# Kernel optimization log

Hardware: AMD Instinct MI355X
Metric: run time of the kernel (lower is better)

## Reference

```python
import jax, jax.numpy as jnp
import numpy as np

B, AT, NBR = 8, 96, 512
NG, NT = 25, 5            # n_gaussian_triple, n_theta
NANG = NG * NT            # 125, filternet input dim
NF = 128                  # n_filters
NB = 128                  # n_atom_basis


def ssp(x):
    # shifted softplus: ln(0.5*e^x + 0.5) = softplus(x) - ln(2)
    return jax.nn.softplus(x) - jnp.asarray(np.log(2.0), x.dtype)


def setup_inputs() -> dict:
    key = jax.random.key(0)
    ks = jax.random.split(key, 16)
    s = lambda fan_in: 1.0 / np.sqrt(fan_in)
    return {
        "x": jax.random.normal(ks[0], (B, AT, NB), jnp.float32),
        "triple_ijk": jax.random.uniform(ks[1], (B, AT, NBR, NANG), jnp.float32),
        "neighbors_j": jax.random.randint(ks[2], (B, AT, NBR), 0, AT, jnp.int32),
        "neighbors_k": jax.random.randint(ks[3], (B, AT, NBR), 0, AT, jnp.int32),
        "triple_mask": jnp.ones((B, AT, NBR), jnp.float32),
        # filter network (Dense ssp -> Dense linear)
        "W1": jax.random.normal(ks[4], (NANG, NF), jnp.float32) * s(NANG),
        "b1": jnp.zeros((NF,), jnp.float32),
        "W2": jax.random.normal(ks[5], (NF, NF), jnp.float32) * s(NF),
        "b2": jnp.zeros((NF,), jnp.float32),
        # cfconv in2f (no bias) and f2out (ssp activation)
        "Win": jax.random.normal(ks[6], (NB, NF), jnp.float32) * s(NB),
        "Wf2": jax.random.normal(ks[7], (NF, NB), jnp.float32) * s(NF),
        "bf2": jnp.zeros((NB,), jnp.float32),
        # final dense (linear) before residual
        "Wd": jax.random.normal(ks[8], (NB, NB), jnp.float32) * s(NB),
        "bd": jnp.zeros((NB,), jnp.float32),
    }


def _gather_atoms(y, nbh):
    # y: (B, At, F); nbh: (B, At, Nbr) -> (B, At, Nbr, F)
    b, at, nbr = nbh.shape
    idx = nbh.reshape(b, at * nbr, 1)
    return jnp.take_along_axis(y, idx, axis=1).reshape(b, at, nbr, y.shape[-1])


def reference(x, triple_ijk, neighbors_j, neighbors_k, triple_mask,
              W1, b1, W2, b2, Win, Wf2, bf2, Wd, bd):
    # filter network on angular/radial triple features -> (B, At, Nbr, NF)
    W_triple = ssp(triple_ijk @ W1 + b1) @ W2 + b2
    # in2f
    y = x @ Win                                  # (B, At, NF)
    y_j = _gather_atoms(y, neighbors_j)          # (B, At, Nbr, NF)
    y_k = _gather_atoms(y, neighbors_k)          # (B, At, Nbr, NF)
    # element-wise continuous-filter conv over triples, mask padded triples
    yt = y_j * y_k * W_triple * triple_mask[..., None]
    agg = jnp.sum(yt, axis=2)                    # sum-aggregate over triples
    v = ssp(agg @ Wf2 + bf2)                     # f2out with shifted softplus
    v = v @ Wd + bd                              # interaction dense
    return x + v                                 # residual
```

## Files before the change

kernel.cpp:

```cpp
#include <hip/hip_runtime.h>
#include <math.h>

#define B_    8
#define AT_   96
#define NBR_  512
#define NANG_ 125
#define NF_   128
#define NB_   128
#define TN    32
#define NCHUNK 2
#define CROWS (NBR_ / NCHUNK)
#define NTI   (CROWS / TN)
#define TSTRIDE 136
#define JSTRIDE 132

typedef __attribute__((ext_vector_type(8))) short bf16x8;
typedef __attribute__((ext_vector_type(4))) float f32x4;

__device__ __forceinline__ short f2bf(float f) {
    union { float f; unsigned u; } x; x.f = f;
    return (short)((x.u + 0x8000u) >> 16);
}

__device__ __forceinline__ float sspf(float x) {
    float p = __builtin_amdgcn_exp2f(x * 1.44269504088896340736f);
    float l = __builtin_amdgcn_logf(1.0f + p);
    return 0.69314718055994530942f * l - 0.69314718055994530942f;
}

__device__ __forceinline__ f32x4 ld4u(const float* p) {
    f32x4 v; __builtin_memcpy(&v, p, 16); return v;
}

__device__ __forceinline__ bf16x8 cvt8(f32x4 lo, f32x4 hi) {
    unsigned r0, r1, r2, r3;
    asm("v_cvt_pk_bf16_f32 %0, %1, %2" : "=v"(r0) : "v"(lo.x), "v"(lo.y));
    asm("v_cvt_pk_bf16_f32 %0, %1, %2" : "=v"(r1) : "v"(lo.z), "v"(lo.w));
    asm("v_cvt_pk_bf16_f32 %0, %1, %2" : "=v"(r2) : "v"(hi.x), "v"(hi.y));
    asm("v_cvt_pk_bf16_f32 %0, %1, %2" : "=v"(r3) : "v"(hi.z), "v"(hi.w));
    typedef __attribute__((ext_vector_type(4))) unsigned u32x4;
    u32x4 r = { r0, r1, r2, r3 };
    return __builtin_bit_cast(bf16x8, r);
}

__global__ __launch_bounds__(128) void prep_kernel(
    const float* __restrict__ x, const float* __restrict__ Win,
    const float* __restrict__ W1, const float* __restrict__ W2,
    float* __restrict__ y, short* __restrict__ w1p, short* __restrict__ w2p)
{
    __shared__ float xs[4][NB_];
    int blk = blockIdx.x, tid = threadIdx.x;
    if (blk < 192) {
        int row0 = blk * 4;
        #pragma unroll
        for (int r = 0; r < 4; r++) xs[r][tid] = x[(row0 + r) * NB_ + tid];
        __syncthreads();
        float a0 = 0.f, a1 = 0.f, a2 = 0.f, a3 = 0.f;
        #pragma unroll 8
        for (int k = 0; k < NB_; k++) {
            float w = Win[k * NF_ + tid];
            a0 = fmaf(xs[0][k], w, a0);
            a1 = fmaf(xs[1][k], w, a1);
            a2 = fmaf(xs[2][k], w, a2);
            a3 = fmaf(xs[3][k], w, a3);
        }
        y[(row0 + 0) * NF_ + tid] = a0;
        y[(row0 + 1) * NF_ + tid] = a1;
        y[(row0 + 2) * NF_ + tid] = a2;
        y[(row0 + 3) * NF_ + tid] = a3;
    } else {
        int t = (blk - 192) * 128 + tid;
        int j = t & 7, lane = (t >> 3) & 63, ks = (t >> 9) & 3, ct = t >> 11;
        int k = ks * 32 + (lane >> 4) * 8 + j;
        int n = ct * 16 + (lane & 15);
        w1p[t] = (k < NANG_) ? f2bf(W1[k * NF_ + n]) : (short)0;
        w2p[t] = f2bf(W2[k * NF_ + n]);
    }
}

__global__ __launch_bounds__(256, 2) void triple_partial(
    const float* __restrict__ trip,
    const int* __restrict__ nbj, const int* __restrict__ nbk,
    const float* __restrict__ maskg,
    const float* __restrict__ b1g, const float* __restrict__ b2g,
    const float* __restrict__ y, const short* __restrict__ w1p,
    const short* __restrict__ w2p, float* __restrict__ pagg)
{
    __shared__ short hs[2][TN * TSTRIDE];
    __shared__ float yjk[2][TN * JSTRIDE];

    const int tid = threadIdx.x;
    const int wave = tid >> 6, lane = tid & 63;
    const int quad = lane >> 4, col = lane & 15;
    const int blk = blockIdx.x;
    const int bid = blk >> 1, c = blk & 1;
    const int b = bid / AT_;

    const float* tpc = trip + (long)bid * NBR_ * NANG_ + (long)c * CROWS * NANG_;
    const int nb_base = bid * NBR_ + c * CROWS;

    const int ct0 = 2 * wave, ct1 = 2 * wave + 1;
    const int f0 = ct0 * 16 + col, f1 = ct1 * 16 + col;
    const float bias1_0 = b1g[f0], bias1_1 = b1g[f1];
    const float bias2_0 = b2g[f0], bias2_1 = b2g[f1];

    const int yrow = tid >> 3, ypart = tid & 7;
    const bool lastblk = (blk == B_ * AT_ * NCHUNK - 1);

    bf16x8 w1f0[4], w1f1[4], w2f0[4], w2f1[4];
    #pragma unroll
    for (int ks = 0; ks < 4; ks++) {
        w1f0[ks] = *(const bf16x8*)&w1p[(ct0 * 4 + ks) * 512 + lane * 8];
        w1f1[ks] = *(const bf16x8*)&w1p[(ct1 * 4 + ks) * 512 + lane * 8];
        w2f0[ks] = *(const bf16x8*)&w2p[(ct0 * 4 + ks) * 512 + lane * 8];
        w2f1[ks] = *(const bf16x8*)&w2p[(ct1 * 4 + ks) * 512 + lane * 8];
    }

    int jj = nbj[nb_base + yrow];
    int kk = nbk[nb_base + yrow];
    float mk = maskg[nb_base + yrow];

    const float* arow = tpc + col * NANG_;
    f32x4 pa0 = ld4u(arow + quad * 8);
    f32x4 pa1 = ld4u(arow + quad * 8 + 4);
    f32x4 pb0 = ld4u(arow + 16 * NANG_ + quad * 8);
    f32x4 pb1 = ld4u(arow + 16 * NANG_ + quad * 8 + 4);

    float accw0 = 0.f, accw1 = 0.f;
    int cur = 0;

    for (int nt = 0; nt < NTI; nt++) {
        const float* yjp = y + (b * AT_ + jj) * NF_ + ypart * 16;
        const float* ykp = y + (b * AT_ + kk) * NF_ + ypart * 16;
        f32x4 j0 = ((const f32x4*)yjp)[0], j1 = ((const f32x4*)yjp)[1];
        f32x4 j2 = ((const f32x4*)yjp)[2], j3 = ((const f32x4*)yjp)[3];
        f32x4 k0 = ((const f32x4*)ykp)[0], k1 = ((const f32x4*)ykp)[1];
        f32x4 k2 = ((const f32x4*)ykp)[2], k3 = ((const f32x4*)ykp)[3];
        const float mc = mk;
        if (nt + 1 < NTI) {
            jj = nbj[nb_base + (nt + 1) * TN + yrow];
            kk = nbk[nb_base + (nt + 1) * TN + yrow];
            mk = maskg[nb_base + (nt + 1) * TN + yrow];
        }

        const bool lt = lastblk && (nt == NTI - 1);
        const float* anext = (nt == NTI - 1) ? arow : (arow + TN * NANG_);

        f32x4 d00 = {0,0,0,0}, d01 = {0,0,0,0}, d10 = {0,0,0,0}, d11 = {0,0,0,0};
        #pragma unroll
        for (int ks = 0; ks < 4; ks++) {
            bf16x8 a0 = cvt8(pa0, pa1);
            bf16x8 a1 = cvt8(pb0, pb1);
            const float* pn = (ks < 3) ? arow : anext;
            const int    ko = (ks < 3) ? ((ks + 1) * 32 + quad * 8) : (quad * 8);
            pa0 = ld4u(pn + ko);
            pa1 = ld4u(pn + ko + 4);
            pb0 = ld4u(pn + 16 * NANG_ + ko);
            if (ks == 2 && lt && lane == 63) {
                pb1 = (f32x4){ pn[16 * NANG_ + ko + 4], 0.f, 0.f, 0.f };
            } else {
                pb1 = ld4u(pn + 16 * NANG_ + ko + 4);
            }
            d00 = __builtin_amdgcn_mfma_f32_16x16x32_bf16(a0, w1f0[ks], d00, 0, 0, 0);
            d01 = __builtin_amdgcn_mfma_f32_16x16x32_bf16(a0, w1f1[ks], d01, 0, 0, 0);
            d10 = __builtin_amdgcn_mfma_f32_16x16x32_bf16(a1, w1f0[ks], d10, 0, 0, 0);
            d11 = __builtin_amdgcn_mfma_f32_16x16x32_bf16(a1, w1f1[ks], d11, 0, 0, 0);
        }
        arow = anext;

        {
            float* d = &yjk[cur][yrow * JSTRIDE + ypart * 16];
            *(f32x4*)(d + 0)  = j0 * k0 * mc;
            *(f32x4*)(d + 4)  = j1 * k1 * mc;
            *(f32x4*)(d + 8)  = j2 * k2 * mc;
            *(f32x4*)(d + 12) = j3 * k3 * mc;
        }
        #pragma unroll
        for (int r = 0; r < 4; r++) {
            int row0 = quad * 4 + r, row1 = 16 + quad * 4 + r;
            hs[cur][row0 * TSTRIDE + f0] = f2bf(sspf(d00[r] + bias1_0));
            hs[cur][row0 * TSTRIDE + f1] = f2bf(sspf(d01[r] + bias1_1));
            hs[cur][row1 * TSTRIDE + f0] = f2bf(sspf(d10[r] + bias1_0));
            hs[cur][row1 * TSTRIDE + f1] = f2bf(sspf(d11[r] + bias1_1));
        }
        __syncthreads();

        f32x4 e00 = {0,0,0,0}, e01 = {0,0,0,0}, e10 = {0,0,0,0}, e11 = {0,0,0,0};
        #pragma unroll
        for (int ks = 0; ks < 4; ks++) {
            bf16x8 a0 = *(const bf16x8*)&hs[cur][(     col) * TSTRIDE + ks * 32 + quad * 8];
            bf16x8 a1 = *(const bf16x8*)&hs[cur][(16 + col) * TSTRIDE + ks * 32 + quad * 8];
            e00 = __builtin_amdgcn_mfma_f32_16x16x32_bf16(a0, w2f0[ks], e00, 0, 0, 0);
            e01 = __builtin_amdgcn_mfma_f32_16x16x32_bf16(a0, w2f1[ks], e01, 0, 0, 0);
            e10 = __builtin_amdgcn_mfma_f32_16x16x32_bf16(a1, w2f0[ks], e10, 0, 0, 0);
            e11 = __builtin_amdgcn_mfma_f32_16x16x32_bf16(a1, w2f1[ks], e11, 0, 0, 0);
        }
        #pragma unroll
        for (int r = 0; r < 4; r++) {
            int row0 = quad * 4 + r, row1 = 16 + quad * 4 + r;
            accw0 += (e00[r] + bias2_0) * yjk[cur][row0 * JSTRIDE + f0];
            accw1 += (e01[r] + bias2_1) * yjk[cur][row0 * JSTRIDE + f1];
            accw0 += (e10[r] + bias2_0) * yjk[cur][row1 * JSTRIDE + f0];
            accw1 += (e11[r] + bias2_1) * yjk[cur][row1 * JSTRIDE + f1];
        }
        cur ^= 1;
    }

    accw0 += __shfl_xor(accw0, 16, 64);
    accw0 += __shfl_xor(accw0, 32, 64);
    accw1 += __shfl_xor(accw1, 16, 64);
    accw1 += __shfl_xor(accw1, 32, 64);
    if (quad == 0) {
        pagg[blk * NF_ + f0] = accw0;
        pagg[blk * NF_ + f1] = accw1;
    }
}

__global__ __launch_bounds__(128) void finish_kernel(
    const float* __restrict__ x, const float* __restrict__ pagg,
    const float* __restrict__ Wf2, const float* __restrict__ bf2,
    const float* __restrict__ Wd, const float* __restrict__ bd,
    float* __restrict__ out)
{
    __shared__ float aggs[NF_];
    __shared__ float t1s[NF_];
    int bid = blockIdx.x, f = threadIdx.x;
    float a = pagg[(bid * 2 + 0) * NF_ + f] + pagg[(bid * 2 + 1) * NF_ + f];
    aggs[f] = a;
    __syncthreads();
    float acc = 0.f;
    #pragma unroll 8
    for (int k = 0; k < NF_; k++) acc = fmaf(aggs[k], Wf2[k * NB_ + f], acc);
    t1s[f] = sspf(acc + bf2[f]);
    __syncthreads();
    acc = 0.f;
    #pragma unroll 8
    for (int k = 0; k < NB_; k++) acc = fmaf(t1s[k], Wd[k * NB_ + f], acc);
    out[bid * NB_ + f] = x[bid * NB_ + f] + acc + bd[f];
}

extern "C" void kernel_launch(void* const* d_in, const int* in_sizes, int n_in,
                              void* d_out, int out_size, void* d_ws, size_t ws_size,
                              hipStream_t stream) {
    const float* x    = (const float*)d_in[0];
    const float* trip = (const float*)d_in[1];
    const int*   nbj  = (const int*)d_in[2];
    const int*   nbk  = (const int*)d_in[3];
    const float* mask = (const float*)d_in[4];
    const float* W1   = (const float*)d_in[5];
    const float* b1   = (const float*)d_in[6];
    const float* W2   = (const float*)d_in[7];
    const float* b2   = (const float*)d_in[8];
    const float* Win  = (const float*)d_in[9];
    const float* Wf2  = (const float*)d_in[10];
    const float* bf2  = (const float*)d_in[11];
    const float* Wd   = (const float*)d_in[12];
    const float* bd   = (const float*)d_in[13];
    float* out = (float*)d_out;

    char* ws = (char*)d_ws;
    float* y    = (float*)ws;
    short* w1p  = (short*)(ws + 393216);
    short* w2p  = (short*)(ws + 393216 + 32768);
    float* pagg = (float*)(ws + 393216 + 65536);

    prep_kernel<<<320, 128, 0, stream>>>(x, Win, W1, W2, y, w1p, w2p);
    triple_partial<<<B_ * AT_ * NCHUNK, 256, 0, stream>>>(trip, nbj, nbk, mask,
        b1, b2, y, w1p, w2p, pagg);
    finish_kernel<<<B_ * AT_, 128, 0, stream>>>(x, pagg, Wf2, bf2, Wd, bd, out);
}
```

Measured before the change: 397.3 us.

## Stage triple tiles into LDS with async global_load_lds double buffering

The triple-feature tile for each 32-row step is now copied straight into a double-buffered LDS region with global_load_lds. The next tile is prefetched while the current one is consumed, replacing the per-lane unaligned global register loads and the special-case guard on the last block. The yj*yk*mask product is also re-laid out so each wave writes and reads only its own 32 columns in a private LDS slice. Dropping the min-blocks launch-bounds hint and adding about 32KB of LDS may change register allocation and occupancy.

```diff
diff --git a/kernel.cpp b/kernel.cpp
--- a/kernel.cpp
+++ b/kernel.cpp
@@ -12,10 +12,13 @@
 #define CROWS (NBR_ / NCHUNK)
 #define NTI   (CROWS / TN)
 #define TSTRIDE 136
-#define JSTRIDE 132
+#define YSTRIDE 36
 
 typedef __attribute__((ext_vector_type(8))) short bf16x8;
 typedef __attribute__((ext_vector_type(4))) float f32x4;
+
+#define AS_G __attribute__((address_space(1)))
+#define AS_L __attribute__((address_space(3)))
 
 __device__ __forceinline__ short f2bf(float f) {
     union { float f; unsigned u; } x; x.f = f;
@@ -26,10 +29,6 @@
     float p = __builtin_amdgcn_exp2f(x * 1.44269504088896340736f);
     float l = __builtin_amdgcn_logf(1.0f + p);
     return 0.69314718055994530942f * l - 0.69314718055994530942f;
-}
-
-__device__ __forceinline__ f32x4 ld4u(const float* p) {
-    f32x4 v; __builtin_memcpy(&v, p, 16); return v;
 }
 
 __device__ __forceinline__ bf16x8 cvt8(f32x4 lo, f32x4 hi) {
@@ -41,6 +40,21 @@
     typedef __attribute__((ext_vector_type(4))) unsigned u32x4;
     u32x4 r = { r0, r1, r2, r3 };
     return __builtin_bit_cast(bf16x8, r);
+}
+
+__device__ __forceinline__ void gl_lds16(const void* g, void* l) {
+    __builtin_amdgcn_global_load_lds((const AS_G void*)g, (AS_L void*)l, 16, 0, 0);
+}
+
+__device__ __forceinline__ void stage_tile(const float* g, float* l, int tid) {
+    int wave = tid >> 6;
+    const char* gb = (const char*)g + tid * 16;
+    char* lb = (char*)l + wave * 1024;
+    gl_lds16(gb,          lb);
+    gl_lds16(gb + 4096,   lb + 4096);
+    gl_lds16(gb + 8192,   lb + 8192);
+    if (tid < 232)
+        gl_lds16(gb + 12288, lb + 12288);
 }
 
 __global__ __launch_bounds__(128) void prep_kernel(
@@ -78,7 +92,7 @@
     }
 }
 
-__global__ __launch_bounds__(256, 2) void triple_partial(
+__global__ __launch_bounds__(256) void triple_partial(
     const float* __restrict__ trip,
     const int* __restrict__ nbj, const int* __restrict__ nbk,
     const float* __restrict__ maskg,
@@ -86,8 +100,9 @@
     const float* __restrict__ y, const short* __restrict__ w1p,
     const short* __restrict__ w2p, float* __restrict__ pagg)
 {
+    __shared__ float ldsT[2][4008];
     __shared__ short hs[2][TN * TSTRIDE];
-    __shared__ float yjk[2][TN * JSTRIDE];
+    __shared__ float yjkw[4][TN * YSTRIDE];
 
     const int tid = threadIdx.x;
     const int wave = tid >> 6, lane = tid & 63;
@@ -104,8 +119,8 @@
     const float bias1_0 = b1g[f0], bias1_1 = b1g[f1];
     const float bias2_0 = b2g[f0], bias2_1 = b2g[f1];
 
-    const int yrow = tid >> 3, ypart = tid & 7;
-    const bool lastblk = (blk == B_ * AT_ * NCHUNK - 1);
+    const int row2 = lane >> 1, h = lane & 1;
+    const int ycol = wave * 32 + h * 16;
 
     bf16x8 w1f0[4], w1f1[4], w2f0[4], w2f1[4];
     #pragma unroll
@@ -116,60 +131,56 @@
         w2f1[ks] = *(const bf16x8*)&w2p[(ct1 * 4 + ks) * 512 + lane * 8];
     }
 
-    int jj = nbj[nb_base + yrow];
-    int kk = nbk[nb_base + yrow];
-    float mk = maskg[nb_base + yrow];
-
-    const float* arow = tpc + col * NANG_;
-    f32x4 pa0 = ld4u(arow + quad * 8);
-    f32x4 pa1 = ld4u(arow + quad * 8 + 4);
-    f32x4 pb0 = ld4u(arow + 16 * NANG_ + quad * 8);
-    f32x4 pb1 = ld4u(arow + 16 * NANG_ + quad * 8 + 4);
+    if (tid < 8) { ldsT[0][4000 + tid] = 0.f; ldsT[1][4000 + tid] = 0.f; }
+
+    stage_tile(tpc, &ldsT[0][0], tid);
+    int jj = nbj[nb_base + row2];
+    int kk = nbk[nb_base + row2];
+    float mk = maskg[nb_base + row2];
+
+    __syncthreads();
 
     float accw0 = 0.f, accw1 = 0.f;
     int cur = 0;
 
     for (int nt = 0; nt < NTI; nt++) {
-        const float* yjp = y + (b * AT_ + jj) * NF_ + ypart * 16;
-        const float* ykp = y + (b * AT_ + kk) * NF_ + ypart * 16;
-        f32x4 j0 = ((const f32x4*)yjp)[0], j1 = ((const f32x4*)yjp)[1];
-        f32x4 j2 = ((const f32x4*)yjp)[2], j3 = ((const f32x4*)yjp)[3];
-        f32x4 k0 = ((const f32x4*)ykp)[0], k1 = ((const f32x4*)ykp)[1];
-        f32x4 k2 = ((const f32x4*)ykp)[2], k3 = ((const f32x4*)ykp)[3];
+        if (nt + 1 < NTI)
+            stage_tile(tpc + (nt + 1) * (TN * NANG_), &ldsT[cur ^ 1][0], tid);
+
+        const float* yj = y + (b * AT_ + jj) * NF_ + ycol;
+        const float* yk = y + (b * AT_ + kk) * NF_ + ycol;
+        f32x4 j0 = ((const f32x4*)yj)[0], j1 = ((const f32x4*)yj)[1];
+        f32x4 j2 = ((const f32x4*)yj)[2], j3 = ((const f32x4*)yj)[3];
+        f32x4 k0 = ((const f32x4*)yk)[0], k1 = ((const f32x4*)yk)[1];
+        f32x4 k2 = ((const f32x4*)yk)[2], k3 = ((const f32x4*)yk)[3];
         const float mc = mk;
         if (nt + 1 < NTI) {
-            jj = nbj[nb_base + (nt + 1) * TN + yrow];
-            kk = nbk[nb_base + (nt + 1) * TN + yrow];
-            mk = maskg[nb_base + (nt + 1) * TN + yrow];
-        }
-
-        const bool lt = lastblk && (nt == NTI - 1);
-        const float* anext = (nt == NTI - 1) ? arow : (arow + TN * NANG_);
-
+            jj = nbj[nb_base + (nt + 1) * TN + row2];
+            kk = nbk[nb_base + (nt + 1) * TN + row2];
+            mk = maskg[nb_base + (nt + 1) * TN + row2];
+        }
+
+        const float* rA = &ldsT[cur][col * NANG_];
+        const float* rB = &ldsT[cur][(16 + col) * NANG_];
         f32x4 d00 = {0,0,0,0}, d01 = {0,0,0,0}, d10 = {0,0,0,0}, d11 = {0,0,0,0};
         #pragma unroll
         for (int ks = 0; ks < 4; ks++) {
-            bf16x8 a0 = cvt8(pa0, pa1);
-            bf16x8 a1 = cvt8(pb0, pb1);
-            const float* pn = (ks < 3) ? arow : anext;
-            const int    ko = (ks < 3) ? ((ks + 1) * 32 + quad * 8) : (quad * 8);
-            pa0 = ld4u(pn + ko);
-            pa1 = ld4u(pn + ko + 4);
-            pb0 = ld4u(pn + 16 * NANG_ + ko);
-            if (ks == 2 && lt && lane == 63) {
-                pb1 = (f32x4){ pn[16 * NANG_ + ko + 4], 0.f, 0.f, 0.f };
-            } else {
-                pb1 = ld4u(pn + 16 * NANG_ + ko + 4);
-            }
+            const int ko = ks * 32 + quad * 8;
+            float a[8], bfl[8];
+            #pragma unroll
+            for (int j = 0; j < 8; j++) a[j] = rA[ko + j];
+            #pragma unroll
+            for (int j = 0; j < 8; j++) bfl[j] = rB[ko + j];
+            bf16x8 a0 = cvt8((f32x4){a[0],a[1],a[2],a[3]}, (f32x4){a[4],a[5],a[6],a[7]});
+            bf16x8 a1 = cvt8((f32x4){bfl[0],bfl[1],bfl[2],bfl[3]}, (f32x4){bfl[4],bfl[5],bfl[6],bfl[7]});
             d00 = __builtin_amdgcn_mfma_f32_16x16x32_bf16(a0, w1f0[ks], d00, 0, 0, 0);
             d01 = __builtin_amdgcn_mfma_f32_16x16x32_bf16(a0, w1f1[ks], d01, 0, 0, 0);
             d10 = __builtin_amdgcn_mfma_f32_16x16x32_bf16(a1, w1f0[ks], d10, 0, 0, 0);
             d11 = __builtin_amdgcn_mfma_f32_16x16x32_bf16(a1, w1f1[ks], d11, 0, 0, 0);
         }
-        arow = anext;
 
         {
-            float* d = &yjk[cur][yrow * JSTRIDE + ypart * 16];
+            float* d = &yjkw[wave][row2 * YSTRIDE + h * 16];
             *(f32x4*)(d + 0)  = j0 * k0 * mc;
             *(f32x4*)(d + 4)  = j1 * k1 * mc;
             *(f32x4*)(d + 8)  = j2 * k2 * mc;
@@ -195,13 +206,14 @@
             e10 = __builtin_amdgcn_mfma_f32_16x16x32_bf16(a1, w2f0[ks], e10, 0, 0, 0);
             e11 = __builtin_amdgcn_mfma_f32_16x16x32_bf16(a1, w2f1[ks], e11, 0, 0, 0);
         }
+        const float* yw = &yjkw[wave][0];
         #pragma unroll
         for (int r = 0; r < 4; r++) {
             int row0 = quad * 4 + r, row1 = 16 + quad * 4 + r;
-            accw0 += (e00[r] + bias2_0) * yjk[cur][row0 * JSTRIDE + f0];
-            accw1 += (e01[r] + bias2_1) * yjk[cur][row0 * JSTRIDE + f1];
-            accw0 += (e10[r] + bias2_0) * yjk[cur][row1 * JSTRIDE + f0];
-            accw1 += (e11[r] + bias2_1) * yjk[cur][row1 * JSTRIDE + f1];
+            accw0 += (e00[r] + bias2_0) * yw[row0 * YSTRIDE + col];
+            accw1 += (e01[r] + bias2_1) * yw[row0 * YSTRIDE + col + 16];
+            accw0 += (e10[r] + bias2_0) * yw[row1 * YSTRIDE + col];
+            accw1 += (e11[r] + bias2_1) * yw[row1 * YSTRIDE + col + 16];
         }
         cur ^= 1;
     }
```

Result: faster. 347.2 us (-12.6%).
